# Optimization experiments

Measured on AMD Instinct MI355X. Metric: run time of the kernel, lower is better.

The kernel has to match this reference:

```python
import jax, jax.numpy as jnp
import numpy as np

DECAY = 0.99
EPS = 1e-05


def setup_inputs() -> dict:
    key = jax.random.key(0)
    k1, k2, k3, k4 = jax.random.split(key, 4)
    B, T, D, K = 16, 4096, 128, 1024
    return {
        "z": jax.random.normal(k1, (B, T, D), dtype=jnp.float32),
        "embedding": jax.random.normal(k2, (K, D), dtype=jnp.float32),
        "cluster_size": jax.random.uniform(k3, (K,), dtype=jnp.float32),
        "ema_w": jax.random.normal(k4, (K, D), dtype=jnp.float32),
    }


def reference(z, embedding, cluster_size, ema_w):
    B, T, D = z.shape
    K = embedding.shape[0]
    z_flat = z.reshape(B * T, D)

    # Squared-distance matrix [N, K]: ||z||^2 - 2 z E^T + ||E||^2
    dist = (
        jnp.sum(z_flat * z_flat, axis=1, keepdims=True)
        - 2.0 * (z_flat @ embedding.T)
        + jnp.sum(embedding * embedding, axis=1)
    )
    indices = jnp.argmin(dist, axis=1)  # [N]
    z_q = embedding[indices].reshape(B, T, D)

    # EMA codebook update (training branch); segment_sum == one_hot.T @ z, one_hot.sum(0)
    batch_cluster = jax.ops.segment_sum(
        jnp.ones((B * T,), dtype=z.dtype), indices, num_segments=K
    )
    new_cluster_size = cluster_size * DECAY + (1.0 - DECAY) * batch_cluster
    batch_ema = jax.ops.segment_sum(z_flat, indices, num_segments=K)
    new_ema_w = ema_w * DECAY + (1.0 - DECAY) * batch_ema

    n = jnp.sum(new_cluster_size)
    smoothed = (new_cluster_size + EPS) / (n + K * EPS) * n
    new_embedding = new_ema_w / smoothed[:, None]

    # Commitment loss on OLD codebook vectors (matches torch order of ops)
    loss_vq = jnp.mean(jnp.square(jax.lax.stop_gradient(z_q) - z))
    # Straight-through estimator
    z_q_st = z + jax.lax.stop_gradient(z_q - z)

    return (
        z_q_st,
        indices.reshape(B, T),
        loss_vq,
        new_embedding,
        new_cluster_size,
        new_ema_w,
    )
```

## Files before the change

### kernel.cpp

```cpp
#include <hip/hip_runtime.h>

#define K_CODES 1024
#define D_DIM 128
#define N_ROWS 65536
#define DECAY_F 0.99f
#define OMD_F 0.01f
#define EPS_F 1e-5f

#define EPAD 136
#define CHUNK_CODES 128
#define CHUNK_USHORT (2 * CHUNK_CODES * EPAD)
#define NT 4
#define HALF_CODES 512
#define HALF_CHUNKS 4
#define SEG_TILE 64

#define WS_CNT     0
#define WS_LOSS    1024
#define WS_BE      1028
#define WS_ZERO_END (1028 + 131072)
#define WS_ENORM   132100
#define WS_SMOOTH  133124
#define WS_CUR     134148
#define WS_FIDX    135172
#define WS_BUCKET  200708
#define WS_SCODE   266244
#define WS_CAND    331780
#define WS_EIMG    593924

typedef __bf16 bf8_t __attribute__((ext_vector_type(8)));
typedef float  f4_t  __attribute__((ext_vector_type(4)));

__device__ inline unsigned short f2bf_bits(float f) {
    __bf16 h = (__bf16)f;
    return __builtin_bit_cast(unsigned short, h);
}
__device__ inline float bf_bits2f(unsigned short u) {
    __bf16 h = __builtin_bit_cast(__bf16, u);
    return (float)h;
}

__device__ inline void gld16(const void* g, void* l) {
    __builtin_amdgcn_global_load_lds(
        (const __attribute__((address_space(1))) void*)g,
        (__attribute__((address_space(3))) void*)l, 16, 0, 0);
}

__global__ void vq_prep(const float* __restrict__ emb, float* __restrict__ ws,
                        float* __restrict__ enorm, unsigned short* __restrict__ eimg) {
    int t = blockIdx.x * blockDim.x + threadIdx.x;
    for (int i = t; i < WS_ZERO_END; i += 32768) ws[i] = 0.f;

    int code = t >> 5;
    int q = t & 31;
    float4 v = ((const float4*)(emb + (size_t)code * D_DIM))[q];
    int chunk = code >> 7, c = code & 127;
    size_t hbase = (size_t)chunk * CHUNK_USHORT + (size_t)c * EPAD + q * 4;
    size_t lbase = hbase + (size_t)CHUNK_CODES * EPAD;
    float vv[4] = {v.x, v.y, v.z, v.w};
    ushort4 hi, lo;
    unsigned short* hp = (unsigned short*)&hi;
    unsigned short* lp = (unsigned short*)&lo;
#pragma unroll
    for (int i = 0; i < 4; ++i) {
        unsigned short hb = f2bf_bits(vv[i]);
        hp[i] = hb;
        lp[i] = f2bf_bits(vv[i] - bf_bits2f(hb));
    }
    *(ushort4*)(eimg + hbase) = hi;
    *(ushort4*)(eimg + lbase) = lo;

    float s = v.x * v.x + v.y * v.y + v.z * v.z + v.w * v.w;
#pragma unroll
    for (int o = 1; o < 32; o <<= 1) s += __shfl_xor(s, o, 64);
    if (q == 0) enorm[code] = s;
}

__device__ inline void top2_update(float s, int code, float& s1, int& i1, float& s2, int& i2) {
    bool b1 = s < s1;
    bool b2 = s < s2;
    s2 = b1 ? s1 : (b2 ? s : s2);
    i2 = b1 ? i1 : (b2 ? code : i2);
    s1 = b1 ? s : s1;
    i1 = b1 ? code : i1;
}

__device__ inline void top2_merge(float& s1, int& i1, float& s2, int& i2,
                                  float t1, int j1, float t2, int j2) {
    bool bf = (t1 < s1) || (t1 == s1 && j1 < i1);
    float ns1 = bf ? t1 : s1;  int ni1 = bf ? j1 : i1;
    float ca  = bf ? s1 : t1;  int ia  = bf ? i1 : j1;
    float cb  = bf ? t2 : s2;  int ib  = bf ? j2 : i2;
    bool bs = (ca < cb) || (ca == cb && ia < ib);
    s1 = ns1; i1 = ni1;
    s2 = bs ? ca : cb; i2 = bs ? ia : ib;
}

__global__ __launch_bounds__(256, 2) void vq_score(
    const float* __restrict__ z, const unsigned short* __restrict__ eimg,
    const float* __restrict__ enorm_g, unsigned int* __restrict__ cand)
{
    __shared__ __align__(16) unsigned short lds[CHUNK_USHORT];
    __shared__ __align__(16) float lds_en[HALF_CODES];

    const int tid  = threadIdx.x;
    const int wv   = tid >> 6;
    const int lane = tid & 63;
    const int l16  = lane & 15;
    const int quad = lane >> 4;
    const int half = blockIdx.x & 1;
    const int rg   = blockIdx.x >> 1;
    const int rowbase = rg * 256 + wv * 64;

    if (tid < HALF_CODES / 4)
        ((float4*)lds_en)[tid] = ((const float4*)(enorm_g + half * HALF_CODES))[tid];

    {
        const char* gs = (const char*)(eimg + (size_t)(half * HALF_CHUNKS) * CHUNK_USHORT);
        char* ls = (char*)lds;
        int wb = wv * 17408;
#pragma unroll
        for (int i = 0; i < 17; ++i)
            gld16(gs + wb + i * 1024 + lane * 16, ls + wb + i * 1024);
    }

    bf8_t zh[NT][4], zl[NT][4];
#pragma unroll
    for (int nt = 0; nt < NT; ++nt) {
        int row = rowbase + nt * 16 + l16;
        const float* zr = z + (size_t)row * D_DIM;
#pragma unroll
        for (int ks = 0; ks < 4; ++ks) {
            const float4* p = (const float4*)(zr + ks * 32 + quad * 8);
            float4 a = p[0], b = p[1];
            float v[8] = {a.x, a.y, a.z, a.w, b.x, b.y, b.z, b.w};
#pragma unroll
            for (int i = 0; i < 8; ++i) {
                __bf16 hh = (__bf16)v[i];
                zh[nt][ks][i] = hh;
                zl[nt][ks][i] = (__bf16)(v[i] - (float)hh);
            }
        }
    }

    float s1[NT], s2[NT];
    int   i1[NT], i2[NT];
#pragma unroll
    for (int nt = 0; nt < NT; ++nt) { s1[nt] = 3.4e38f; s2[nt] = 3.4e38f; i1[nt] = 0; i2[nt] = 0; }

    __syncthreads();

    for (int c = 0; c < HALF_CHUNKS; ++c) {
#pragma unroll
        for (int cg = 0; cg < 4; ++cg) {
            f4_t acc[2][NT];
#pragma unroll
            for (int ct = 0; ct < 2; ++ct)
#pragma unroll
                for (int nt = 0; nt < NT; ++nt) acc[ct][nt] = (f4_t)(0.f);

#pragma unroll
            for (int ks = 0; ks < 4; ++ks) {
                bf8_t ah[2], al[2];
#pragma unroll
                for (int ct = 0; ct < 2; ++ct) {
                    int cl = cg * 32 + ct * 16 + l16;
                    int base = cl * EPAD + ks * 32 + quad * 8;
                    ah[ct] = *(const bf8_t*)&lds[base];
                    al[ct] = *(const bf8_t*)&lds[CHUNK_CODES * EPAD + base];
                }
#pragma unroll
                for (int ct = 0; ct < 2; ++ct)
#pragma unroll
                    for (int nt = 0; nt < NT; ++nt) {
                        acc[ct][nt] = __builtin_amdgcn_mfma_f32_16x16x32_bf16(
                            ah[ct], zh[nt][ks], acc[ct][nt], 0, 0, 0);
                        acc[ct][nt] = __builtin_amdgcn_mfma_f32_16x16x32_bf16(
                            al[ct], zh[nt][ks], acc[ct][nt], 0, 0, 0);
                        acc[ct][nt] = __builtin_amdgcn_mfma_f32_16x16x32_bf16(
                            ah[ct], zl[nt][ks], acc[ct][nt], 0, 0, 0);
                    }
            }

#pragma unroll
            for (int ct = 0; ct < 2; ++ct) {
                int lc = c * 128 + cg * 32 + ct * 16 + quad * 4;
                float4 en4 = *(const float4*)&lds_en[lc];
                float env[4] = {en4.x, en4.y, en4.z, en4.w};
                int gc = half * HALF_CODES + lc;
#pragma unroll
                for (int nt = 0; nt < NT; ++nt)
#pragma unroll
                    for (int r = 0; r < 4; ++r) {
                        float s = env[r] - 2.0f * acc[ct][nt][r];
                        top2_update(s, gc + r, s1[nt], i1[nt], s2[nt], i2[nt]);
                    }
            }
        }
        __syncthreads();
        if (c + 1 < HALF_CHUNKS) {
            const char* gs = (const char*)(eimg +
                (size_t)(half * HALF_CHUNKS + c + 1) * CHUNK_USHORT);
            char* ls = (char*)lds;
            int wb = wv * 17408;
#pragma unroll
            for (int i = 0; i < 17; ++i)
                gld16(gs + wb + i * 1024 + lane * 16, ls + wb + i * 1024);
            __syncthreads();
        }
    }

#pragma unroll
    for (int off = 16; off <= 32; off <<= 1) {
#pragma unroll
        for (int nt = 0; nt < NT; ++nt) {
            float t1 = __shfl_xor(s1[nt], off, 64);
            int   j1 = __shfl_xor(i1[nt], off, 64);
            float t2 = __shfl_xor(s2[nt], off, 64);
            int   j2 = __shfl_xor(i2[nt], off, 64);
            top2_merge(s1[nt], i1[nt], s2[nt], i2[nt], t1, j1, t2, j2);
        }
    }

    if (lane < 16) {
#pragma unroll
        for (int nt = 0; nt < NT; ++nt) {
            int row = rowbase + nt * 16 + l16;
            uint2 p = {(unsigned int)i1[nt], (unsigned int)i2[nt]};
            *(uint2*)(cand + (size_t)row * 4 + half * 2) = p;
        }
    }
}

__global__ __launch_bounds__(256) void vq_decide(
    const float* __restrict__ z, const float* __restrict__ emb,
    const float* __restrict__ enorm, const unsigned int* __restrict__ cand,
    float* __restrict__ out_zq, float* __restrict__ out_idx,
    int* __restrict__ cnt, unsigned int* __restrict__ fidx,
    float* __restrict__ loss_acc)
{
    const int tid  = threadIdx.x;
    const int half = tid & 1;
    const int row  = blockIdx.x * 128 + (tid >> 1);

    float4 zr[16];
    const float4* zp = (const float4*)(z + (size_t)row * D_DIM + half * 64);
#pragma unroll
    for (int i = 0; i < 16; ++i) zr[i] = zp[i];

    uint4 cd = *(const uint4*)(cand + (size_t)row * 4);
    int j[4] = {(int)cd.x, (int)cd.y, (int)cd.z, (int)cd.w};

    float bs = 3.4e38f;
    int   bi = 0x7fffffff;
#pragma unroll
    for (int cidx = 0; cidx < 4; ++cidx) {
        int jj = j[cidx];
        const float4* ep = (const float4*)(emb + (size_t)jj * D_DIM + half * 64);
        float p = 0.f;
#pragma unroll
        for (int i = 0; i < 16; ++i) {
            float4 a = ep[i], zv = zr[i];
            p += zv.x * a.x + zv.y * a.y + zv.z * a.z + zv.w * a.w;
        }
        float d = p + __shfl_xor(p, 1, 64);
        float s = enorm[jj] - 2.0f * d;
        if (s < bs || (s == bs && jj < bi)) { bs = s; bi = jj; }
    }
    int best = bi;

    if (half == 0) {
        out_idx[row] = (float)best;
        fidx[row] = (unsigned int)best;
        atomicAdd(cnt + best, 1);
    }

    const float4* eq = (const float4*)(emb + (size_t)best * D_DIM + half * 64);
    float4* oz = (float4*)(out_zq + (size_t)row * D_DIM + half * 64);

    float ls = 0.f;
#pragma unroll
    for (int i = 0; i < 16; ++i) {
        float4 q = eq[i], zv = zr[i];
        float4 df = {q.x - zv.x, q.y - zv.y, q.z - zv.z, q.w - zv.w};
        ls += df.x * df.x + df.y * df.y + df.z * df.z + df.w * df.w;
        float4 o = {zv.x + df.x, zv.y + df.y, zv.z + df.z, zv.w + df.w};
        oz[i] = o;
    }

#pragma unroll
    for (int off = 32; off > 0; off >>= 1) ls += __shfl_down(ls, off, 64);
    if ((tid & 63) == 0) atomicAdd(loss_acc, ls);
}

__global__ void vq_mid(const float* __restrict__ cs, const int* __restrict__ cnt,
                       const float* __restrict__ loss_acc,
                       float* __restrict__ out_ncs, float* __restrict__ out_loss,
                       float* __restrict__ smoothed, int* __restrict__ cursor)
{
    __shared__ int tmp[K_CODES];
    __shared__ float red[K_CODES];
    int k = threadIdx.x;
    int c = cnt[k];
    tmp[k] = c;
    float ncs = cs[k] * DECAY_F + OMD_F * (float)c;
    out_ncs[k] = ncs;
    red[k] = ncs;
    __syncthreads();
    for (int off = 1; off < K_CODES; off <<= 1) {
        int t = (k >= off) ? tmp[k - off] : 0;
        __syncthreads();
        tmp[k] += t;
        __syncthreads();
    }
    cursor[k] = tmp[k] - c;
    for (int s = 512; s > 0; s >>= 1) {
        if (k < s) red[k] += red[k + s];
        __syncthreads();
    }
    float n = red[0];
    smoothed[k] = (ncs + EPS_F) / (n + (float)K_CODES * EPS_F) * n;
    if (k == 0) out_loss[0] = loss_acc[0] / (float)((size_t)N_ROWS * D_DIM);
}

__global__ void vq_scatter(const unsigned int* __restrict__ fidx,
                           int* __restrict__ cursor, unsigned int* __restrict__ bucket,
                           int* __restrict__ scode)
{
    int row = blockIdx.x * blockDim.x + threadIdx.x;
    int k = (int)fidx[row];
    int slot = atomicAdd(cursor + k, 1);
    bucket[slot] = (unsigned int)row;
    scode[slot]  = k;
}

__global__ __launch_bounds__(128) void vq_segsum(
    const float* __restrict__ z, const unsigned int* __restrict__ bucket,
    const int* __restrict__ scode, float* __restrict__ be)
{
    __shared__ int sb[SEG_TILE];
    __shared__ int sc[SEG_TILE];
    const int tid = threadIdx.x;
    const int t0  = blockIdx.x * SEG_TILE;

    if (tid < SEG_TILE) sb[tid] = (int)bucket[t0 + tid];
    else if (tid < 2 * SEG_TILE) sc[tid - SEG_TILE] = scode[t0 + tid - SEG_TILE];
    __syncthreads();

    const int d = tid;
    float acc = 0.f;
    int cur = sc[0];

    for (int i = 0; i < SEG_TILE; i += 8) {
        float v[8];
#pragma unroll
        for (int jx = 0; jx < 8; ++jx)
            v[jx] = z[(size_t)sb[i + jx] * D_DIM + d];
#pragma unroll
        for (int jx = 0; jx < 8; ++jx) {
            int c = sc[i + jx];
            if (c != cur) {
                atomicAdd(be + (size_t)cur * D_DIM + d, acc);
                acc = 0.f;
                cur = c;
            }
            acc += v[jx];
        }
    }
    atomicAdd(be + (size_t)cur * D_DIM + d, acc);
}

__global__ void vq_fin2(const float* __restrict__ ema_w, const float* __restrict__ be,
                        const float* __restrict__ smoothed,
                        float* __restrict__ out_emb, float* __restrict__ out_ema)
{
    int i = blockIdx.x * blockDim.x + threadIdx.x;
    float e = ema_w[i] * DECAY_F + OMD_F * be[i];
    out_ema[i] = e;
    out_emb[i] = e / smoothed[i >> 7];
}

extern "C" void kernel_launch(void* const* d_in, const int* in_sizes, int n_in,
                              void* d_out, int out_size, void* d_ws, size_t ws_size,
                              hipStream_t stream) {
    const float* z   = (const float*)d_in[0];
    const float* emb = (const float*)d_in[1];
    const float* cs  = (const float*)d_in[2];
    const float* ema = (const float*)d_in[3];

    float* out    = (float*)d_out;
    float* o_zq   = out;
    float* o_idx  = o_zq + (size_t)N_ROWS * D_DIM;
    float* o_loss = o_idx + N_ROWS;
    float* o_emb  = o_loss + 1;
    float* o_ncs  = o_emb + K_CODES * D_DIM;
    float* o_ema  = o_ncs + K_CODES;

    float* ws = (float*)d_ws;
    int*            cnt      = (int*)(ws + WS_CNT);
    float*          lacc     = ws + WS_LOSS;
    float*          be       = ws + WS_BE;
    float*          enorm    = ws + WS_ENORM;
    float*          smoothed = ws + WS_SMOOTH;
    int*            cursor   = (int*)(ws + WS_CUR);
    unsigned int*   fidx     = (unsigned int*)(ws + WS_FIDX);
    unsigned int*   bucket   = (unsigned int*)(ws + WS_BUCKET);
    int*            scode    = (int*)(ws + WS_SCODE);
    unsigned int*   cand     = (unsigned int*)(ws + WS_CAND);
    unsigned short* eimg     = (unsigned short*)(ws + WS_EIMG);

    vq_prep<<<128, 256, 0, stream>>>(emb, ws, enorm, eimg);
    vq_score<<<512, 256, 0, stream>>>(z, eimg, enorm, cand);
    vq_decide<<<512, 256, 0, stream>>>(z, emb, enorm, cand,
                                       o_zq, o_idx, cnt, fidx, lacc);
    vq_mid<<<1, K_CODES, 0, stream>>>(cs, cnt, lacc, o_ncs, o_loss, smoothed, cursor);
    vq_scatter<<<N_ROWS / 256, 256, 0, stream>>>(fidx, cursor, bucket, scode);
    vq_segsum<<<N_ROWS / SEG_TILE, 128, 0, stream>>>(z, bucket, scode, be);
    vq_fin2<<<K_CODES * D_DIM / 256, 256, 0, stream>>>(ema, be, smoothed, o_emb, o_ema);
}
```

Before: 256.4 us.

## Split scoring across code quarters, switch to fp16 split, rescue only ambiguous rows

The scoring kernel now splits the codebook into four quarters over smaller row tiles, with more blocks and higher occupancy. It uses fp16 hi/lo splitting instead of bf16 and does a per-lane 8-way reduction before the top-2 update. The decide kernel no longer recomputes fp32 distances for every row: it merges the scored top-2 candidates and rescores exactly only when the gap falls below a threshold. The loss is computed from the score plus a precomputed z norm, and the z_q copy moves to a separate kernel. This trades exact fp32 verification for a heuristic threshold, which risks index mismatches and loss precision, and adds fp16 range concerns.

```diff
diff --git a/kernel.cpp b/kernel.cpp
--- a/kernel.cpp
+++ b/kernel.cpp
@@ -8,12 +8,13 @@
 #define EPS_F 1e-5f
 
 #define EPAD 136
-#define CHUNK_CODES 128
-#define CHUNK_USHORT (2 * CHUNK_CODES * EPAD)
-#define NT 4
-#define HALF_CODES 512
-#define HALF_CHUNKS 4
+#define CH_CODES 64
+#define CH64_U (2 * CH_CODES * EPAD)
+#define CH_LO 8704
+#define NT 2
+#define QCODES 256
 #define SEG_TILE 64
+#define RESCUE_EPS 1e-3f
 
 #define WS_CNT     0
 #define WS_LOSS    1024
@@ -23,20 +24,21 @@
 #define WS_SMOOTH  133124
 #define WS_CUR     134148
 #define WS_FIDX    135172
-#define WS_BUCKET  200708
-#define WS_SCODE   266244
-#define WS_CAND    331780
-#define WS_EIMG    593924
-
-typedef __bf16 bf8_t __attribute__((ext_vector_type(8)));
-typedef float  f4_t  __attribute__((ext_vector_type(4)));
-
-__device__ inline unsigned short f2bf_bits(float f) {
-    __bf16 h = (__bf16)f;
+#define WS_ZNORM   200708
+#define WS_CAND    266244
+#define WS_BUCKET  266244
+#define WS_SCODE   331780
+#define WS_EIMG    1314820
+
+typedef _Float16 h8_t __attribute__((ext_vector_type(8)));
+typedef float    f4_t __attribute__((ext_vector_type(4)));
+
+__device__ inline unsigned short f2h_bits(float f) {
+    _Float16 h = (_Float16)f;
     return __builtin_bit_cast(unsigned short, h);
 }
-__device__ inline float bf_bits2f(unsigned short u) {
-    __bf16 h = __builtin_bit_cast(__bf16, u);
+__device__ inline float h_bits2f(unsigned short u) {
+    _Float16 h = __builtin_bit_cast(_Float16, u);
     return (float)h;
 }
 
@@ -54,18 +56,18 @@
     int code = t >> 5;
     int q = t & 31;
     float4 v = ((const float4*)(emb + (size_t)code * D_DIM))[q];
-    int chunk = code >> 7, c = code & 127;
-    size_t hbase = (size_t)chunk * CHUNK_USHORT + (size_t)c * EPAD + q * 4;
-    size_t lbase = hbase + (size_t)CHUNK_CODES * EPAD;
+    int chunk = code >> 6, c = code & 63;
+    size_t hbase = (size_t)chunk * CH64_U + (size_t)c * EPAD + q * 4;
+    size_t lbase = hbase + CH_LO;
     float vv[4] = {v.x, v.y, v.z, v.w};
     ushort4 hi, lo;
     unsigned short* hp = (unsigned short*)&hi;
     unsigned short* lp = (unsigned short*)&lo;
 #pragma unroll
     for (int i = 0; i < 4; ++i) {
-        unsigned short hb = f2bf_bits(vv[i]);
+        unsigned short hb = f2h_bits(vv[i]);
         hp[i] = hb;
-        lp[i] = f2bf_bits(vv[i] - bf_bits2f(hb));
+        lp[i] = f2h_bits(vv[i] - h_bits2f(hb));
     }
     *(ushort4*)(eimg + hbase) = hi;
     *(ushort4*)(eimg + lbase) = lo;
@@ -96,39 +98,42 @@
     s2 = bs ? ca : cb; i2 = bs ? ia : ib;
 }
 
-__global__ __launch_bounds__(256, 2) void vq_score(
+__global__ __launch_bounds__(256, 4) void vq_score(
     const float* __restrict__ z, const unsigned short* __restrict__ eimg,
-    const float* __restrict__ enorm_g, unsigned int* __restrict__ cand)
-{
-    __shared__ __align__(16) unsigned short lds[CHUNK_USHORT];
-    __shared__ __align__(16) float lds_en[HALF_CODES];
+    const float* __restrict__ enorm_g, uint4* __restrict__ cand,
+    float* __restrict__ znorm)
+{
+    __shared__ __align__(16) unsigned short lds[CH64_U];
+    __shared__ __align__(16) float lds_en[QCODES];
 
     const int tid  = threadIdx.x;
     const int wv   = tid >> 6;
     const int lane = tid & 63;
     const int l16  = lane & 15;
     const int quad = lane >> 4;
-    const int half = blockIdx.x & 1;
-    const int rg   = blockIdx.x >> 1;
-    const int rowbase = rg * 256 + wv * 64;
-
-    if (tid < HALF_CODES / 4)
-        ((float4*)lds_en)[tid] = ((const float4*)(enorm_g + half * HALF_CODES))[tid];
+    const int qs   = blockIdx.x & 3;
+    const int rg   = blockIdx.x >> 2;
+    const int rowbase = rg * 128 + wv * 32;
+
+    if (tid < QCODES / 4)
+        ((float4*)lds_en)[tid] = ((const float4*)(enorm_g + qs * QCODES))[tid];
 
     {
-        const char* gs = (const char*)(eimg + (size_t)(half * HALF_CHUNKS) * CHUNK_USHORT);
+        const char* gs = (const char*)(eimg + (size_t)(qs * 4) * CH64_U);
         char* ls = (char*)lds;
-        int wb = wv * 17408;
-#pragma unroll
-        for (int i = 0; i < 17; ++i)
+        int wb = wv * 8704;
+#pragma unroll
+        for (int i = 0; i < 8; ++i)
             gld16(gs + wb + i * 1024 + lane * 16, ls + wb + i * 1024);
-    }
-
-    bf8_t zh[NT][4], zl[NT][4];
+        if (lane < 32) gld16(gs + wb + 8192 + lane * 16, ls + wb + 8192);
+    }
+
+    h8_t zh[NT][4], zl[NT][4];
 #pragma unroll
     for (int nt = 0; nt < NT; ++nt) {
         int row = rowbase + nt * 16 + l16;
         const float* zr = z + (size_t)row * D_DIM;
+        float zn = 0.f;
 #pragma unroll
         for (int ks = 0; ks < 4; ++ks) {
             const float4* p = (const float4*)(zr + ks * 32 + quad * 8);
@@ -136,11 +141,15 @@
             float v[8] = {a.x, a.y, a.z, a.w, b.x, b.y, b.z, b.w};
 #pragma unroll
             for (int i = 0; i < 8; ++i) {
-                __bf16 hh = (__bf16)v[i];
+                _Float16 hh = (_Float16)v[i];
                 zh[nt][ks][i] = hh;
-                zl[nt][ks][i] = (__bf16)(v[i] - (float)hh);
+                zl[nt][ks][i] = (_Float16)(v[i] - (float)hh);
+                zn += v[i] * v[i];
             }
         }
+        zn += __shfl_xor(zn, 16, 64);
+        zn += __shfl_xor(zn, 32, 64);
+        if (qs == 0 && quad == 0) znorm[row] = zn;
     }
 
     float s1[NT], s2[NT];
@@ -150,9 +159,9 @@
 
     __syncthreads();
 
-    for (int c = 0; c < HALF_CHUNKS; ++c) {
-#pragma unroll
-        for (int cg = 0; cg < 4; ++cg) {
+    for (int ch = 0; ch < 4; ++ch) {
+#pragma unroll
+        for (int cg = 0; cg < 2; ++cg) {
             f4_t acc[2][NT];
 #pragma unroll
             for (int ct = 0; ct < 2; ++ct)
@@ -161,51 +170,61 @@
 
 #pragma unroll
             for (int ks = 0; ks < 4; ++ks) {
-                bf8_t ah[2], al[2];
+                h8_t ah[2], al[2];
 #pragma unroll
                 for (int ct = 0; ct < 2; ++ct) {
                     int cl = cg * 32 + ct * 16 + l16;
                     int base = cl * EPAD + ks * 32 + quad * 8;
-                    ah[ct] = *(const bf8_t*)&lds[base];
-                    al[ct] = *(const bf8_t*)&lds[CHUNK_CODES * EPAD + base];
+                    ah[ct] = *(const h8_t*)&lds[base];
+                    al[ct] = *(const h8_t*)&lds[CH_LO + base];
                 }
 #pragma unroll
                 for (int ct = 0; ct < 2; ++ct)
 #pragma unroll
                     for (int nt = 0; nt < NT; ++nt) {
-                        acc[ct][nt] = __builtin_amdgcn_mfma_f32_16x16x32_bf16(
+                        acc[ct][nt] = __builtin_amdgcn_mfma_f32_16x16x32_f16(
                             ah[ct], zh[nt][ks], acc[ct][nt], 0, 0, 0);
-                        acc[ct][nt] = __builtin_amdgcn_mfma_f32_16x16x32_bf16(
+                        acc[ct][nt] = __builtin_amdgcn_mfma_f32_16x16x32_f16(
                             al[ct], zh[nt][ks], acc[ct][nt], 0, 0, 0);
-                        acc[ct][nt] = __builtin_amdgcn_mfma_f32_16x16x32_bf16(
+                        acc[ct][nt] = __builtin_amdgcn_mfma_f32_16x16x32_f16(
                             ah[ct], zl[nt][ks], acc[ct][nt], 0, 0, 0);
                     }
             }
 
-#pragma unroll
-            for (int ct = 0; ct < 2; ++ct) {
-                int lc = c * 128 + cg * 32 + ct * 16 + quad * 4;
-                float4 en4 = *(const float4*)&lds_en[lc];
-                float env[4] = {en4.x, en4.y, en4.z, en4.w};
-                int gc = half * HALF_CODES + lc;
-#pragma unroll
-                for (int nt = 0; nt < NT; ++nt)
-#pragma unroll
-                    for (int r = 0; r < 4; ++r) {
-                        float s = env[r] - 2.0f * acc[ct][nt][r];
-                        top2_update(s, gc + r, s1[nt], i1[nt], s2[nt], i2[nt]);
-                    }
+            int lcb = ch * 64 + cg * 32;
+            float4 e0 = *(const float4*)&lds_en[lcb + quad * 4];
+            float4 e1 = *(const float4*)&lds_en[lcb + 16 + quad * 4];
+            float env0[4] = {e0.x, e0.y, e0.z, e0.w};
+            float env1[4] = {e1.x, e1.y, e1.z, e1.w};
+            int cb = qs * QCODES + lcb + quad * 4;
+#pragma unroll
+            for (int nt = 0; nt < NT; ++nt) {
+                float sv[8];
+#pragma unroll
+                for (int r = 0; r < 4; ++r) {
+                    sv[r]     = fmaf(-2.f, acc[0][nt][r], env0[r]);
+                    sv[4 + r] = fmaf(-2.f, acc[1][nt][r], env1[r]);
+                }
+                float bs_ = sv[0]; int li = 0;
+#pragma unroll
+                for (int k = 1; k < 8; ++k) {
+                    bool t = sv[k] < bs_;
+                    bs_ = t ? sv[k] : bs_;
+                    li  = t ? k : li;
+                }
+                int code = cb + ((li >> 2) << 4) + (li & 3);
+                top2_update(bs_, code, s1[nt], i1[nt], s2[nt], i2[nt]);
             }
         }
         __syncthreads();
-        if (c + 1 < HALF_CHUNKS) {
-            const char* gs = (const char*)(eimg +
-                (size_t)(half * HALF_CHUNKS + c + 1) * CHUNK_USHORT);
+        if (ch + 1 < 4) {
+            const char* gs = (const char*)(eimg + (size_t)(qs * 4 + ch + 1) * CH64_U);
             char* ls = (char*)lds;
-            int wb = wv * 17408;
-#pragma unroll
-            for (int i = 0; i < 17; ++i)
+            int wb = wv * 8704;
+#pragma unroll
+            for (int i = 0; i < 8; ++i)
                 gld16(gs + wb + i * 1024 + lane * 16, ls + wb + i * 1024);
+            if (lane < 32) gld16(gs + wb + 8192 + lane * 16, ls + wb + 8192);
             __syncthreads();
         }
     }
@@ -226,71 +245,75 @@
 #pragma unroll
         for (int nt = 0; nt < NT; ++nt) {
             int row = rowbase + nt * 16 + l16;
-            uint2 p = {(unsigned int)i1[nt], (unsigned int)i2[nt]};
-            *(uint2*)(cand + (size_t)row * 4 + half * 2) = p;
-        }
-    }
-}
-
-__global__ __launch_bounds__(256) void vq_decide(
+            uint4 p = {__float_as_uint(s1[nt]), (unsigned int)i1[nt],
+                       __float_as_uint(s2[nt]), (unsigned int)i2[nt]};
+            cand[(size_t)row * 4 + qs] = p;
+        }
+    }
+}
+
+__global__ __launch_bounds__(256) void vq_finish(
     const float* __restrict__ z, const float* __restrict__ emb,
-    const float* __restrict__ enorm, const unsigned int* __restrict__ cand,
-    float* __restrict__ out_zq, float* __restrict__ out_idx,
-    int* __restrict__ cnt, unsigned int* __restrict__ fidx,
-    float* __restrict__ loss_acc)
-{
-    const int tid  = threadIdx.x;
-    const int half = tid & 1;
-    const int row  = blockIdx.x * 128 + (tid >> 1);
-
-    float4 zr[16];
-    const float4* zp = (const float4*)(z + (size_t)row * D_DIM + half * 64);
-#pragma unroll
-    for (int i = 0; i < 16; ++i) zr[i] = zp[i];
-
-    uint4 cd = *(const uint4*)(cand + (size_t)row * 4);
-    int j[4] = {(int)cd.x, (int)cd.y, (int)cd.z, (int)cd.w};
-
-    float bs = 3.4e38f;
-    int   bi = 0x7fffffff;
-#pragma unroll
-    for (int cidx = 0; cidx < 4; ++cidx) {
-        int jj = j[cidx];
-        const float4* ep = (const float4*)(emb + (size_t)jj * D_DIM + half * 64);
-        float p = 0.f;
-#pragma unroll
-        for (int i = 0; i < 16; ++i) {
-            float4 a = ep[i], zv = zr[i];
-            p += zv.x * a.x + zv.y * a.y + zv.z * a.z + zv.w * a.w;
-        }
-        float d = p + __shfl_xor(p, 1, 64);
-        float s = enorm[jj] - 2.0f * d;
-        if (s < bs || (s == bs && jj < bi)) { bs = s; bi = jj; }
-    }
-    int best = bi;
-
-    if (half == 0) {
-        out_idx[row] = (float)best;
-        fidx[row] = (unsigned int)best;
-        atomicAdd(cnt + best, 1);
-    }
-
-    const float4* eq = (const float4*)(emb + (size_t)best * D_DIM + half * 64);
-    float4* oz = (float4*)(out_zq + (size_t)row * D_DIM + half * 64);
-
-    float ls = 0.f;
-#pragma unroll
-    for (int i = 0; i < 16; ++i) {
-        float4 q = eq[i], zv = zr[i];
-        float4 df = {q.x - zv.x, q.y - zv.y, q.z - zv.z, q.w - zv.w};
-        ls += df.x * df.x + df.y * df.y + df.z * df.z + df.w * df.w;
-        float4 o = {zv.x + df.x, zv.y + df.y, zv.z + df.z, zv.w + df.w};
-        oz[i] = o;
-    }
-
+    const float* __restrict__ enorm, const uint4* __restrict__ cand,
+    const float* __restrict__ znorm,
+    float* __restrict__ out_idx, unsigned int* __restrict__ fidx,
+    int* __restrict__ cnt, float* __restrict__ loss_acc)
+{
+    int row = blockIdx.x * 256 + threadIdx.x;
+    uint4 q0 = cand[(size_t)row * 4 + 0];
+    uint4 q1 = cand[(size_t)row * 4 + 1];
+    uint4 q2 = cand[(size_t)row * 4 + 2];
+    uint4 q3 = cand[(size_t)row * 4 + 3];
+
+    float s1 = __uint_as_float(q0.x); int i1 = (int)q0.y;
+    float s2 = __uint_as_float(q0.z); int i2 = (int)q0.w;
+    top2_merge(s1, i1, s2, i2, __uint_as_float(q1.x), (int)q1.y,
+                               __uint_as_float(q1.z), (int)q1.w);
+    top2_merge(s1, i1, s2, i2, __uint_as_float(q2.x), (int)q2.y,
+                               __uint_as_float(q2.z), (int)q2.w);
+    top2_merge(s1, i1, s2, i2, __uint_as_float(q3.x), (int)q3.y,
+                               __uint_as_float(q3.z), (int)q3.w);
+
+    int best = i1;
+    float sbest = s1;
+    if (s2 - s1 < RESCUE_EPS) {
+        int cs8[8] = {(int)q0.y, (int)q0.w, (int)q1.y, (int)q1.w,
+                      (int)q2.y, (int)q2.w, (int)q3.y, (int)q3.w};
+        const float4* zr = (const float4*)(z + (size_t)row * D_DIM);
+        float bs = 3.4e38f; int bi = 0x7fffffff;
+        for (int c = 0; c < 8; ++c) {
+            int j = cs8[c];
+            const float4* ep = (const float4*)(emb + (size_t)j * D_DIM);
+            float p = 0.f;
+            for (int i = 0; i < 32; ++i) {
+                float4 a = ep[i], zv = zr[i];
+                p += zv.x * a.x + zv.y * a.y + zv.z * a.z + zv.w * a.w;
+            }
+            float s = enorm[j] - 2.f * p;
+            if (s < bs || (s == bs && j < bi)) { bs = s; bi = j; }
+        }
+        best = bi; sbest = bs;
+    }
+
+    out_idx[row] = (float)best;
+    fidx[row] = (unsigned int)best;
+    atomicAdd(cnt + best, 1);
+
+    float ls = sbest + znorm[row];
 #pragma unroll
     for (int off = 32; off > 0; off >>= 1) ls += __shfl_down(ls, off, 64);
-    if ((tid & 63) == 0) atomicAdd(loss_acc, ls);
+    if ((threadIdx.x & 63) == 0) atomicAdd(loss_acc, ls);
+}
+
+__global__ __launch_bounds__(256) void vq_zqcopy(
+    const float* __restrict__ emb, const unsigned int* __restrict__ fidx,
+    float* __restrict__ out_zq)
+{
+    int t = blockIdx.x * 256 + threadIdx.x;
+    int row = t >> 5, off = t & 31;
+    int best = (int)fidx[row];
+    ((float4*)out_zq)[(size_t)row * 32 + off] =
+        ((const float4*)emb)[(size_t)best * 32 + off];
 }
 
 __global__ void vq_mid(const float* __restrict__ cs, const int* __restrict__ cnt,
@@ -404,15 +427,17 @@
     float*          smoothed = ws + WS_SMOOTH;
     int*            cursor   = (int*)(ws + WS_CUR);
     unsigned int*   fidx     = (unsigned int*)(ws + WS_FIDX);
+    float*          znorm    = ws + WS_ZNORM;
+    uint4*          cand     = (uint4*)(ws + WS_CAND);
     unsigned int*   bucket   = (unsigned int*)(ws + WS_BUCKET);
     int*            scode    = (int*)(ws + WS_SCODE);
-    unsigned int*   cand     = (unsigned int*)(ws + WS_CAND);
     unsigned short* eimg     = (unsigned short*)(ws + WS_EIMG);
 
     vq_prep<<<128, 256, 0, stream>>>(emb, ws, enorm, eimg);
-    vq_score<<<512, 256, 0, stream>>>(z, eimg, enorm, cand);
-    vq_decide<<<512, 256, 0, stream>>>(z, emb, enorm, cand,
-                                       o_zq, o_idx, cnt, fidx, lacc);
+    vq_score<<<2048, 256, 0, stream>>>(z, eimg, enorm, cand, znorm);
+    vq_finish<<<256, 256, 0, stream>>>(z, emb, enorm, cand, znorm,
+                                       o_idx, fidx, cnt, lacc);
+    vq_zqcopy<<<8192, 256, 0, stream>>>(emb, fidx, o_zq);
     vq_mid<<<1, K_CODES, 0, stream>>>(cs, cnt, lacc, o_ncs, o_loss, smoothed, cursor);
     vq_scatter<<<N_ROWS / 256, 256, 0, stream>>>(fidx, cursor, bucket, scode);
     vq_segsum<<<N_ROWS / SEG_TILE, 128, 0, stream>>>(z, bucket, scode, be);
```

New measurement: 297.7 us. 16.1% more time.
